# Optimization experiments

Measured on AMD Instinct MI355X. Metric: run time of the kernel, lower is better.

## Reference

```python
import jax, jax.numpy as jnp
import numpy as np

N_INPUTS = 4
ACTIVE_IDX = 0
HIDDEN = 2048
EPS = 1e-6
ROUTER_INPUT_SCALE = float(HIDDEN ** (-1.0))


def _rms_norm(x, w, eps=EPS):
    var = jnp.mean(jnp.square(x), axis=-1, keepdims=True)
    return x * jax.lax.rsqrt(var + eps) * w


def _modalities(x, w_norm, W_router):
    # tanh(router(norm(x) * hidden_size**-1)) -> [B, S, n]
    r = _rms_norm(x, w_norm) * ROUTER_INPUT_SCALE
    return jnp.tanh(r @ W_router.T)


def setup_inputs() -> dict:
    key = jax.random.key(0)
    k0, k1, k2, k3, k4 = jax.random.split(key, 5)
    B, S = 2, 4096
    return {
        "hidden_states": jax.random.normal(k0, (N_INPUTS, B, S, HIDDEN), jnp.float32),
        "activated": jax.random.normal(k1, (B, S, HIDDEN), jnp.float32),
        "w_norm": jnp.ones((HIDDEN,), jnp.float32),
        "W_router": jax.random.normal(k2, (N_INPUTS, HIDDEN), jnp.float32) * 0.02,
        "W_pred": jax.random.normal(k3, (N_INPUTS * N_INPUTS, N_INPUTS), jnp.float32) * 0.02,
        "W_corr": jax.random.normal(k4, (N_INPUTS, N_INPUTS), jnp.float32) * 0.02,
    }


def reference(hidden_states, activated, w_norm, W_router, W_pred, W_corr):
    n = N_INPUTS
    # ---- predict ----
    active = hidden_states[ACTIVE_IDX]                      # [B,S,H]
    mods = _modalities(active, w_norm, W_router)            # [B,S,n]
    coefs = (mods @ W_pred.T)                               # [B,S,n*n]
    coefs = coefs.reshape(*coefs.shape[:-1], n, n)          # [B,S,n,n]
    coefs = jnp.swapaxes(coefs, -1, -2)                     # transpose last two dims
    stacked = jnp.moveaxis(hidden_states, 0, -1)            # [B,S,H,n]
    preds = jnp.einsum('bshk,bskj->bshj', stacked, coefs) + stacked
    predictions = jnp.moveaxis(preds, -1, 0)                # [n,B,S,H]
    # ---- correct ----
    mods_c = _modalities(activated, w_norm, W_router)       # [B,S,n]
    innovation = activated - predictions[ACTIVE_IDX]        # [B,S,H]
    ccoefs = mods_c @ W_corr.T + 1.0                        # [B,S,n]
    corrected = predictions + innovation[None] * jnp.moveaxis(ccoefs, -1, 0)[..., None]
    return corrected                                        # [n,B,S,H]
```

## Files before the change

### kernel.cpp

```cpp
#include <hip/hip_runtime.h>


constexpr int H = 2048;
constexpr float EPS = 1e-6f;

__global__ __launch_bounds__(512) void altup_fused(
    const float* __restrict__ hs,
    const float* __restrict__ act,
    const float* __restrict__ w_norm,
    const float* __restrict__ W_router,
    const float* __restrict__ W_pred,
    const float* __restrict__ W_corr,
    float* __restrict__ out,
    long long T)
{
    const long long t = blockIdx.x;
    const int tid = threadIdx.x;
    const long long row = t * (long long)H;
    const long long plane = T * (long long)H;
    const int h = tid * 4;

    __shared__ float s_red[8][10];

    const float4 x0 = *reinterpret_cast<const float4*>(hs + row + h);
    const float4 x1 = *reinterpret_cast<const float4*>(hs + plane + row + h);
    const float4 x2 = *reinterpret_cast<const float4*>(hs + 2 * plane + row + h);
    const float4 x3 = *reinterpret_cast<const float4*>(hs + 3 * plane + row + h);
    const float4 xc = *reinterpret_cast<const float4*>(act + row + h);
    const float4 wn = *reinterpret_cast<const float4*>(w_norm + h);

    float p[10];
    {
        const float* a = &x0.x;
        const float* c = &xc.x;
        const float* w = &wn.x;
        float s0 = 0.f, s5 = 0.f;
#pragma unroll
        for (int e = 0; e < 4; ++e) { s0 += a[e] * a[e]; s5 += c[e] * c[e]; }
        p[0] = s0; p[5] = s5;
#pragma unroll
        for (int i = 0; i < 4; ++i) {
            const float4 wr4 = *reinterpret_cast<const float4*>(W_router + i * H + h);
            const float* r = &wr4.x;
            float da = 0.f, dc = 0.f;
#pragma unroll
            for (int e = 0; e < 4; ++e) {
                const float wre = w[e] * r[e];
                da += a[e] * wre;
                dc += c[e] * wre;
            }
            p[1 + i] = da; p[6 + i] = dc;
        }
    }

#pragma unroll
    for (int m = 1; m < 64; m <<= 1) {
#pragma unroll
        for (int i = 0; i < 10; ++i) p[i] += __shfl_xor(p[i], m, 64);
    }
    const int wave = tid >> 6;
    if ((tid & 63) == 0) {
#pragma unroll
        for (int i = 0; i < 10; ++i) s_red[wave][i] = p[i];
    }
    __syncthreads();

    float tot[10];
#pragma unroll
    for (int i = 0; i < 10; ++i) {
        float s = 0.f;
#pragma unroll
        for (int wv = 0; wv < 8; ++wv) s += s_red[wv][i];
        tot[i] = s;
    }

    const float ris = 1.0f / (float)H;
    const float inv_a = rsqrtf(tot[0] * ris + EPS) * ris;
    const float inv_c = rsqrtf(tot[5] * ris + EPS) * ris;
    float mods[4], modsc[4];
#pragma unroll
    for (int i = 0; i < 4; ++i) {
        mods[i]  = tanhf(tot[1 + i] * inv_a);
        modsc[i] = tanhf(tot[6 + i] * inv_c);
    }
    float coefT[4][4];
#pragma unroll
    for (int j = 0; j < 4; ++j)
#pragma unroll
        for (int k = 0; k < 4; ++k) {
            float s = 0.f;
#pragma unroll
            for (int m = 0; m < 4; ++m) s += mods[m] * W_pred[(j * 4 + k) * 4 + m];
            coefT[k][j] = s;
        }
    float ccoef[4];
#pragma unroll
    for (int j = 0; j < 4; ++j) {
        float s = 1.0f;
#pragma unroll
        for (int m = 0; m < 4; ++m) s += modsc[m] * W_corr[j * 4 + m];
        ccoef[j] = s;
    }

    const float* xk0 = &x0.x;
    const float* xk1 = &x1.x;
    const float* xk2 = &x2.x;
    const float* xk3 = &x3.x;
    const float* xce = &xc.x;
    float4 o4[4];
#pragma unroll
    for (int e = 0; e < 4; ++e) {
        const float xk[4] = { xk0[e], xk1[e], xk2[e], xk3[e] };
        float pred[4];
#pragma unroll
        for (int j = 0; j < 4; ++j) {
            float s = xk[j];
#pragma unroll
            for (int k = 0; k < 4; ++k) s += xk[k] * coefT[k][j];
            pred[j] = s;
        }
        const float innov = xce[e] - pred[0];
#pragma unroll
        for (int j = 0; j < 4; ++j)
            (&o4[j].x)[e] = pred[j] + innov * ccoef[j];
    }
#pragma unroll
    for (int j = 0; j < 4; ++j)
        *reinterpret_cast<float4*>(out + j * plane + row + h) = o4[j];
}

extern "C" void kernel_launch(void* const* d_in, const int* in_sizes, int n_in,
                              void* d_out, int out_size, void* d_ws, size_t ws_size,
                              hipStream_t stream) {
    const float* hs       = (const float*)d_in[0];
    const float* act      = (const float*)d_in[1];
    const float* w_norm   = (const float*)d_in[2];
    const float* W_router = (const float*)d_in[3];
    const float* W_pred   = (const float*)d_in[4];
    const float* W_corr   = (const float*)d_in[5];
    float* out = (float*)d_out;
    const long long T = (long long)in_sizes[0] / (4LL * H);
    altup_fused<<<dim3((unsigned)T), dim3(512), 0, stream>>>(
        hs, act, w_norm, W_router, W_pred, W_corr, out, T);
}
```

Before: 121.4 us.

## Split fused kernel into coefficient pass and streaming apply pass with nontemporal access

Splits the single fused kernel into two. The first computes per-token router coefficients into workspace, reading only the active plane and the activated tensor. The second streams all four planes, using nontemporal loads for planes 1-3 and nontemporal stores for the output. The intent is to keep the apply kernel lightweight and free of barriers so it runs at full bandwidth. The cost is a second launch and re-reading the active plane and activated tensor, about two extra tensor reads. The fused kernel remains as a fallback when the workspace is too small.

```diff
diff --git a/kernel.cpp b/kernel.cpp
--- a/kernel.cpp
+++ b/kernel.cpp
@@ -4,13 +4,108 @@
 constexpr int H = 2048;
 constexpr float EPS = 1e-6f;
 
-__global__ __launch_bounds__(512) void altup_fused(
+typedef float f32x4 __attribute__((ext_vector_type(4)));
+
+__global__ __launch_bounds__(512) void altup_coefs(
     const float* __restrict__ hs,
     const float* __restrict__ act,
     const float* __restrict__ w_norm,
     const float* __restrict__ W_router,
     const float* __restrict__ W_pred,
     const float* __restrict__ W_corr,
+    float* __restrict__ coefs)
+{
+    const long long t = blockIdx.x;
+    const int tid = threadIdx.x;
+    const long long row = t * (long long)H;
+    const int h = tid * 4;
+
+    __shared__ float s_red[8][10];
+
+    const f32x4 xa = *reinterpret_cast<const f32x4*>(hs + row + h);
+    const f32x4 xc = *reinterpret_cast<const f32x4*>(act + row + h);
+    const f32x4 wn = *reinterpret_cast<const f32x4*>(w_norm + h);
+
+    float p[10];
+    {
+        float s0 = 0.f, s5 = 0.f;
+#pragma unroll
+        for (int e = 0; e < 4; ++e) { s0 += xa[e] * xa[e]; s5 += xc[e] * xc[e]; }
+        p[0] = s0; p[5] = s5;
+#pragma unroll
+        for (int i = 0; i < 4; ++i) {
+            const f32x4 wr4 = *reinterpret_cast<const f32x4*>(W_router + i * H + h);
+            float da = 0.f, dc = 0.f;
+#pragma unroll
+            for (int e = 0; e < 4; ++e) {
+                const float wre = wn[e] * wr4[e];
+                da += xa[e] * wre;
+                dc += xc[e] * wre;
+            }
+            p[1 + i] = da; p[6 + i] = dc;
+        }
+    }
+
+#pragma unroll
+    for (int m = 1; m < 64; m <<= 1) {
+#pragma unroll
+        for (int i = 0; i < 10; ++i) p[i] += __shfl_xor(p[i], m, 64);
+    }
+    const int wave = tid >> 6;
+    if ((tid & 63) == 0) {
+#pragma unroll
+        for (int i = 0; i < 10; ++i) s_red[wave][i] = p[i];
+    }
+    __syncthreads();
+    if (tid != 0) return;
+
+    float tot[10];
+#pragma unroll
+    for (int i = 0; i < 10; ++i) {
+        float s = 0.f;
+#pragma unroll
+        for (int wv = 0; wv < 8; ++wv) s += s_red[wv][i];
+        tot[i] = s;
+    }
+
+    const float ris = 1.0f / (float)H;
+    const float inv_a = rsqrtf(tot[0] * ris + EPS) * ris;
+    const float inv_c = rsqrtf(tot[5] * ris + EPS) * ris;
+    float mods[4], modsc[4];
+#pragma unroll
+    for (int i = 0; i < 4; ++i) {
+        mods[i]  = tanhf(tot[1 + i] * inv_a);
+        modsc[i] = tanhf(tot[6 + i] * inv_c);
+    }
+    float cf[20];
+#pragma unroll
+    for (int k = 0; k < 4; ++k)
+#pragma unroll
+        for (int j = 0; j < 4; ++j) {
+            float s = 0.f;
+#pragma unroll
+            for (int m = 0; m < 4; ++m) s += mods[m] * W_pred[(j * 4 + k) * 4 + m];
+            cf[k * 4 + j] = s;
+        }
+#pragma unroll
+    for (int j = 0; j < 4; ++j) {
+        float s = 1.0f;
+#pragma unroll
+        for (int m = 0; m < 4; ++m) s += modsc[m] * W_corr[j * 4 + m];
+        cf[16 + j] = s;
+    }
+    float* dst = coefs + t * 20;
+#pragma unroll
+    for (int q = 0; q < 5; ++q) {
+        f32x4 v = { cf[q * 4], cf[q * 4 + 1], cf[q * 4 + 2], cf[q * 4 + 3] };
+        *reinterpret_cast<f32x4*>(dst + q * 4) = v;
+    }
+}
+
+__global__ __launch_bounds__(512) void altup_apply(
+    const float* __restrict__ hs,
+    const float* __restrict__ act,
+    const float* __restrict__ coefs,
     float* __restrict__ out,
     long long T)
 {
@@ -20,39 +115,80 @@
     const long long plane = T * (long long)H;
     const int h = tid * 4;
 
+    const f32x4 x0 = *reinterpret_cast<const f32x4*>(hs + row + h);
+    const f32x4 x1 = __builtin_nontemporal_load(
+        reinterpret_cast<const f32x4*>(hs + plane + row + h));
+    const f32x4 x2 = __builtin_nontemporal_load(
+        reinterpret_cast<const f32x4*>(hs + 2 * plane + row + h));
+    const f32x4 x3 = __builtin_nontemporal_load(
+        reinterpret_cast<const f32x4*>(hs + 3 * plane + row + h));
+    const f32x4 xc = *reinterpret_cast<const f32x4*>(act + row + h);
+
+    const float* cf = coefs + t * 20;
+    float coefT[16], ccoef[4];
+#pragma unroll
+    for (int i = 0; i < 16; ++i) coefT[i] = cf[i];
+#pragma unroll
+    for (int j = 0; j < 4; ++j) ccoef[j] = cf[16 + j];
+
+    f32x4 o4[4];
+#pragma unroll
+    for (int e = 0; e < 4; ++e) {
+        const float xk[4] = { x0[e], x1[e], x2[e], x3[e] };
+        float pred[4];
+#pragma unroll
+        for (int j = 0; j < 4; ++j) {
+            float s = xk[j];
+#pragma unroll
+            for (int k = 0; k < 4; ++k) s += xk[k] * coefT[k * 4 + j];
+            pred[j] = s;
+        }
+        const float innov = xc[e] - pred[0];
+#pragma unroll
+        for (int j = 0; j < 4; ++j)
+            o4[j][e] = pred[j] + innov * ccoef[j];
+    }
+#pragma unroll
+    for (int j = 0; j < 4; ++j)
+        __builtin_nontemporal_store(o4[j],
+            reinterpret_cast<f32x4*>(out + j * plane + row + h));
+}
+
+__global__ __launch_bounds__(512) void altup_fused(
+    const float* __restrict__ hs, const float* __restrict__ act,
+    const float* __restrict__ w_norm, const float* __restrict__ W_router,
+    const float* __restrict__ W_pred, const float* __restrict__ W_corr,
+    float* __restrict__ out, long long T)
+{
+    const long long t = blockIdx.x;
+    const int tid = threadIdx.x;
+    const long long row = t * (long long)H;
+    const long long plane = T * (long long)H;
+    const int h = tid * 4;
     __shared__ float s_red[8][10];
 
-    const float4 x0 = *reinterpret_cast<const float4*>(hs + row + h);
-    const float4 x1 = *reinterpret_cast<const float4*>(hs + plane + row + h);
-    const float4 x2 = *reinterpret_cast<const float4*>(hs + 2 * plane + row + h);
-    const float4 x3 = *reinterpret_cast<const float4*>(hs + 3 * plane + row + h);
-    const float4 xc = *reinterpret_cast<const float4*>(act + row + h);
-    const float4 wn = *reinterpret_cast<const float4*>(w_norm + h);
+    const f32x4 x0 = *reinterpret_cast<const f32x4*>(hs + row + h);
+    const f32x4 x1 = *reinterpret_cast<const f32x4*>(hs + plane + row + h);
+    const f32x4 x2 = *reinterpret_cast<const f32x4*>(hs + 2 * plane + row + h);
+    const f32x4 x3 = *reinterpret_cast<const f32x4*>(hs + 3 * plane + row + h);
+    const f32x4 xc = *reinterpret_cast<const f32x4*>(act + row + h);
+    const f32x4 wn = *reinterpret_cast<const f32x4*>(w_norm + h);
 
     float p[10];
     {
-        const float* a = &x0.x;
-        const float* c = &xc.x;
-        const float* w = &wn.x;
         float s0 = 0.f, s5 = 0.f;
 #pragma unroll
-        for (int e = 0; e < 4; ++e) { s0 += a[e] * a[e]; s5 += c[e] * c[e]; }
+        for (int e = 0; e < 4; ++e) { s0 += x0[e]*x0[e]; s5 += xc[e]*xc[e]; }
         p[0] = s0; p[5] = s5;
 #pragma unroll
         for (int i = 0; i < 4; ++i) {
-            const float4 wr4 = *reinterpret_cast<const float4*>(W_router + i * H + h);
-            const float* r = &wr4.x;
+            const f32x4 wr4 = *reinterpret_cast<const f32x4*>(W_router + i * H + h);
             float da = 0.f, dc = 0.f;
 #pragma unroll
-            for (int e = 0; e < 4; ++e) {
-                const float wre = w[e] * r[e];
-                da += a[e] * wre;
-                dc += c[e] * wre;
-            }
-            p[1 + i] = da; p[6 + i] = dc;
-        }
-    }
-
+            for (int e = 0; e < 4; ++e) { const float wre = wn[e]*wr4[e]; da += x0[e]*wre; dc += xc[e]*wre; }
+            p[1+i] = da; p[6+i] = dc;
+        }
+    }
 #pragma unroll
     for (int m = 1; m < 64; m <<= 1) {
 #pragma unroll
@@ -64,7 +200,6 @@
         for (int i = 0; i < 10; ++i) s_red[wave][i] = p[i];
     }
     __syncthreads();
-
     float tot[10];
 #pragma unroll
     for (int i = 0; i < 10; ++i) {
@@ -73,16 +208,12 @@
         for (int wv = 0; wv < 8; ++wv) s += s_red[wv][i];
         tot[i] = s;
     }
-
     const float ris = 1.0f / (float)H;
     const float inv_a = rsqrtf(tot[0] * ris + EPS) * ris;
     const float inv_c = rsqrtf(tot[5] * ris + EPS) * ris;
     float mods[4], modsc[4];
 #pragma unroll
-    for (int i = 0; i < 4; ++i) {
-        mods[i]  = tanhf(tot[1 + i] * inv_a);
-        modsc[i] = tanhf(tot[6 + i] * inv_c);
-    }
+    for (int i = 0; i < 4; ++i) { mods[i] = tanhf(tot[1+i]*inv_a); modsc[i] = tanhf(tot[6+i]*inv_c); }
     float coefT[4][4];
 #pragma unroll
     for (int j = 0; j < 4; ++j)
@@ -90,7 +221,7 @@
         for (int k = 0; k < 4; ++k) {
             float s = 0.f;
 #pragma unroll
-            for (int m = 0; m < 4; ++m) s += mods[m] * W_pred[(j * 4 + k) * 4 + m];
+            for (int m = 0; m < 4; ++m) s += mods[m] * W_pred[(j*4+k)*4 + m];
             coefT[k][j] = s;
         }
     float ccoef[4];
@@ -98,19 +229,13 @@
     for (int j = 0; j < 4; ++j) {
         float s = 1.0f;
 #pragma unroll
-        for (int m = 0; m < 4; ++m) s += modsc[m] * W_corr[j * 4 + m];
+        for (int m = 0; m < 4; ++m) s += modsc[m] * W_corr[j*4 + m];
         ccoef[j] = s;
     }
-
-    const float* xk0 = &x0.x;
-    const float* xk1 = &x1.x;
-    const float* xk2 = &x2.x;
-    const float* xk3 = &x3.x;
-    const float* xce = &xc.x;
-    float4 o4[4];
+    f32x4 o4[4];
 #pragma unroll
     for (int e = 0; e < 4; ++e) {
-        const float xk[4] = { xk0[e], xk1[e], xk2[e], xk3[e] };
+        const float xk[4] = { x0[e], x1[e], x2[e], x3[e] };
         float pred[4];
 #pragma unroll
         for (int j = 0; j < 4; ++j) {
@@ -119,14 +244,13 @@
             for (int k = 0; k < 4; ++k) s += xk[k] * coefT[k][j];
             pred[j] = s;
         }
-        const float innov = xce[e] - pred[0];
-#pragma unroll
-        for (int j = 0; j < 4; ++j)
-            (&o4[j].x)[e] = pred[j] + innov * ccoef[j];
+        const float innov = xc[e] - pred[0];
+#pragma unroll
+        for (int j = 0; j < 4; ++j) o4[j][e] = pred[j] + innov * ccoef[j];
     }
 #pragma unroll
     for (int j = 0; j < 4; ++j)
-        *reinterpret_cast<float4*>(out + j * plane + row + h) = o4[j];
+        *reinterpret_cast<f32x4*>(out + j * plane + row + h) = o4[j];
 }
 
 extern "C" void kernel_launch(void* const* d_in, const int* in_sizes, int n_in,
@@ -140,6 +264,16 @@
     const float* W_corr   = (const float*)d_in[5];
     float* out = (float*)d_out;
     const long long T = (long long)in_sizes[0] / (4LL * H);
-    altup_fused<<<dim3((unsigned)T), dim3(512), 0, stream>>>(
-        hs, act, w_norm, W_router, W_pred, W_corr, out, T);
-}
+
+    const size_t need = (size_t)T * 20 * sizeof(float);
+    if (ws_size >= need) {
+        float* coefs = (float*)d_ws;
+        altup_coefs<<<dim3((unsigned)T), dim3(512), 0, stream>>>(
+            hs, act, w_norm, W_router, W_pred, W_corr, coefs);
+        altup_apply<<<dim3((unsigned)T), dim3(512), 0, stream>>>(
+            hs, act, coefs, out, T);
+    } else {
+        altup_fused<<<dim3((unsigned)T), dim3(512), 0, stream>>>(
+            hs, act, w_norm, W_router, W_pred, W_corr, out, T);
+    }
+}
```

Result: slower. 144.4 us (+19.0%).

## Process multiple rows per block with register prefetch and nontemporal memory ops

Applied to the files above, without the earlier changes.

Each block now loops over four rows strided by the grid size, prefetching the next row's five input vectors into registers while computing the current one. Router weights premultiplied by the norm weight are loaded once per block. Streaming loads and stores use nontemporal hints to avoid cache pollution. This costs more registers and fewer blocks, which may reduce latency hiding on an already bandwidth-bound kernel.

```diff
diff --git a/kernel.cpp b/kernel.cpp
--- a/kernel.cpp
+++ b/kernel.cpp
@@ -3,6 +3,15 @@
 
 constexpr int H = 2048;
 constexpr float EPS = 1e-6f;
+
+typedef float f32x4 __attribute__((ext_vector_type(4)));
+
+__device__ __forceinline__ f32x4 nt_load(const float* p) {
+    return __builtin_nontemporal_load(reinterpret_cast<const f32x4*>(p));
+}
+__device__ __forceinline__ void nt_store(float* p, f32x4 v) {
+    __builtin_nontemporal_store(v, reinterpret_cast<f32x4*>(p));
+}
 
 __global__ __launch_bounds__(512) void altup_fused(
     const float* __restrict__ hs,
@@ -12,121 +21,135 @@
     const float* __restrict__ W_pred,
     const float* __restrict__ W_corr,
     float* __restrict__ out,
-    long long T)
+    long long T, int iters)
 {
-    const long long t = blockIdx.x;
     const int tid = threadIdx.x;
-    const long long row = t * (long long)H;
+    const int h = tid * 4;
     const long long plane = T * (long long)H;
-    const int h = tid * 4;
+    const long long strideT = gridDim.x;
 
-    __shared__ float s_red[8][10];
+    __shared__ float s_red[2][8][10];
 
-    const float4 x0 = *reinterpret_cast<const float4*>(hs + row + h);
-    const float4 x1 = *reinterpret_cast<const float4*>(hs + plane + row + h);
-    const float4 x2 = *reinterpret_cast<const float4*>(hs + 2 * plane + row + h);
-    const float4 x3 = *reinterpret_cast<const float4*>(hs + 3 * plane + row + h);
-    const float4 xc = *reinterpret_cast<const float4*>(act + row + h);
-    const float4 wn = *reinterpret_cast<const float4*>(w_norm + h);
+    const f32x4 wn = *reinterpret_cast<const f32x4*>(w_norm + h);
+    f32x4 wrw[4];
+#pragma unroll
+    for (int i = 0; i < 4; ++i) {
+        const f32x4 wr = *reinterpret_cast<const f32x4*>(W_router + i * H + h);
+#pragma unroll
+        for (int e = 0; e < 4; ++e) wrw[i][e] = wn[e] * wr[e];
+    }
 
-    float p[10];
-    {
-        const float* a = &x0.x;
-        const float* c = &xc.x;
-        const float* w = &wn.x;
-        float s0 = 0.f, s5 = 0.f;
+    long long t = blockIdx.x;
+
+    f32x4 cx0 = nt_load(hs + t * H + h);
+    f32x4 cx1 = nt_load(hs + plane + t * H + h);
+    f32x4 cx2 = nt_load(hs + 2 * plane + t * H + h);
+    f32x4 cx3 = nt_load(hs + 3 * plane + t * H + h);
+    f32x4 cxc = nt_load(act + t * H + h);
+
+    for (int it = 0; it < iters; ++it) {
+        const long long tn = t + strideT;
+        f32x4 nx0, nx1, nx2, nx3, nxc;
+        if (it + 1 < iters) {
+            nx0 = nt_load(hs + tn * H + h);
+            nx1 = nt_load(hs + plane + tn * H + h);
+            nx2 = nt_load(hs + 2 * plane + tn * H + h);
+            nx3 = nt_load(hs + 3 * plane + tn * H + h);
+            nxc = nt_load(act + tn * H + h);
+        }
+
+        float p[10];
+        {
+            float s0 = 0.f, s5 = 0.f;
 #pragma unroll
-        for (int e = 0; e < 4; ++e) { s0 += a[e] * a[e]; s5 += c[e] * c[e]; }
-        p[0] = s0; p[5] = s5;
+            for (int e = 0; e < 4; ++e) { s0 += cx0[e] * cx0[e]; s5 += cxc[e] * cxc[e]; }
+            p[0] = s0; p[5] = s5;
+#pragma unroll
+            for (int i = 0; i < 4; ++i) {
+                float da = 0.f, dc = 0.f;
+#pragma unroll
+                for (int e = 0; e < 4; ++e) {
+                    da += cx0[e] * wrw[i][e];
+                    dc += cxc[e] * wrw[i][e];
+                }
+                p[1 + i] = da; p[6 + i] = dc;
+            }
+        }
+
+#pragma unroll
+        for (int m = 1; m < 64; m <<= 1) {
+#pragma unroll
+            for (int i = 0; i < 10; ++i) p[i] += __shfl_xor(p[i], m, 64);
+        }
+        const int buf = it & 1;
+        const int wave = tid >> 6;
+        if ((tid & 63) == 0) {
+#pragma unroll
+            for (int i = 0; i < 10; ++i) s_red[buf][wave][i] = p[i];
+        }
+        __syncthreads();
+
+        float tot[10];
+#pragma unroll
+        for (int i = 0; i < 10; ++i) {
+            float s = 0.f;
+#pragma unroll
+            for (int wv = 0; wv < 8; ++wv) s += s_red[buf][wv][i];
+            tot[i] = s;
+        }
+
+        const float ris = 1.0f / (float)H;
+        const float inv_a = rsqrtf(tot[0] * ris + EPS) * ris;
+        const float inv_c = rsqrtf(tot[5] * ris + EPS) * ris;
+        float mods[4], modsc[4];
 #pragma unroll
         for (int i = 0; i < 4; ++i) {
-            const float4 wr4 = *reinterpret_cast<const float4*>(W_router + i * H + h);
-            const float* r = &wr4.x;
-            float da = 0.f, dc = 0.f;
+            mods[i]  = tanhf(tot[1 + i] * inv_a);
+            modsc[i] = tanhf(tot[6 + i] * inv_c);
+        }
+        float coefT[4][4];
 #pragma unroll
-            for (int e = 0; e < 4; ++e) {
-                const float wre = w[e] * r[e];
-                da += a[e] * wre;
-                dc += c[e] * wre;
+        for (int j = 0; j < 4; ++j)
+#pragma unroll
+            for (int k = 0; k < 4; ++k) {
+                float s = 0.f;
+#pragma unroll
+                for (int m = 0; m < 4; ++m) s += mods[m] * W_pred[(j * 4 + k) * 4 + m];
+                coefT[k][j] = s;
             }
-            p[1 + i] = da; p[6 + i] = dc;
-        }
-    }
-
-#pragma unroll
-    for (int m = 1; m < 64; m <<= 1) {
-#pragma unroll
-        for (int i = 0; i < 10; ++i) p[i] += __shfl_xor(p[i], m, 64);
-    }
-    const int wave = tid >> 6;
-    if ((tid & 63) == 0) {
-#pragma unroll
-        for (int i = 0; i < 10; ++i) s_red[wave][i] = p[i];
-    }
-    __syncthreads();
-
-    float tot[10];
-#pragma unroll
-    for (int i = 0; i < 10; ++i) {
-        float s = 0.f;
-#pragma unroll
-        for (int wv = 0; wv < 8; ++wv) s += s_red[wv][i];
-        tot[i] = s;
-    }
-
-    const float ris = 1.0f / (float)H;
-    const float inv_a = rsqrtf(tot[0] * ris + EPS) * ris;
-    const float inv_c = rsqrtf(tot[5] * ris + EPS) * ris;
-    float mods[4], modsc[4];
-#pragma unroll
-    for (int i = 0; i < 4; ++i) {
-        mods[i]  = tanhf(tot[1 + i] * inv_a);
-        modsc[i] = tanhf(tot[6 + i] * inv_c);
-    }
-    float coefT[4][4];
-#pragma unroll
-    for (int j = 0; j < 4; ++j)
-#pragma unroll
-        for (int k = 0; k < 4; ++k) {
-            float s = 0.f;
-#pragma unroll
-            for (int m = 0; m < 4; ++m) s += mods[m] * W_pred[(j * 4 + k) * 4 + m];
-            coefT[k][j] = s;
-        }
-    float ccoef[4];
-#pragma unroll
-    for (int j = 0; j < 4; ++j) {
-        float s = 1.0f;
-#pragma unroll
-        for (int m = 0; m < 4; ++m) s += modsc[m] * W_corr[j * 4 + m];
-        ccoef[j] = s;
-    }
-
-    const float* xk0 = &x0.x;
-    const float* xk1 = &x1.x;
-    const float* xk2 = &x2.x;
-    const float* xk3 = &x3.x;
-    const float* xce = &xc.x;
-    float4 o4[4];
-#pragma unroll
-    for (int e = 0; e < 4; ++e) {
-        const float xk[4] = { xk0[e], xk1[e], xk2[e], xk3[e] };
-        float pred[4];
+        float ccoef[4];
 #pragma unroll
         for (int j = 0; j < 4; ++j) {
-            float s = xk[j];
+            float s = 1.0f;
 #pragma unroll
-            for (int k = 0; k < 4; ++k) s += xk[k] * coefT[k][j];
-            pred[j] = s;
+            for (int m = 0; m < 4; ++m) s += modsc[m] * W_corr[j * 4 + m];
+            ccoef[j] = s;
         }
-        const float innov = xce[e] - pred[0];
+
+        f32x4 o4[4];
+#pragma unroll
+        for (int e = 0; e < 4; ++e) {
+            const float xk[4] = { cx0[e], cx1[e], cx2[e], cx3[e] };
+            float pred[4];
+#pragma unroll
+            for (int j = 0; j < 4; ++j) {
+                float s = xk[j];
+#pragma unroll
+                for (int k = 0; k < 4; ++k) s += xk[k] * coefT[k][j];
+                pred[j] = s;
+            }
+            const float innov = cxc[e] - pred[0];
+#pragma unroll
+            for (int j = 0; j < 4; ++j)
+                o4[j][e] = pred[j] + innov * ccoef[j];
+        }
 #pragma unroll
         for (int j = 0; j < 4; ++j)
-            (&o4[j].x)[e] = pred[j] + innov * ccoef[j];
+            nt_store(out + j * plane + t * H + h, o4[j]);
+
+        t = tn;
+        cx0 = nx0; cx1 = nx1; cx2 = nx2; cx3 = nx3; cxc = nxc;
     }
-#pragma unroll
-    for (int j = 0; j < 4; ++j)
-        *reinterpret_cast<float4*>(out + j * plane + row + h) = o4[j];
 }
 
 extern "C" void kernel_launch(void* const* d_in, const int* in_sizes, int n_in,
@@ -140,6 +163,10 @@
     const float* W_corr   = (const float*)d_in[5];
     float* out = (float*)d_out;
     const long long T = (long long)in_sizes[0] / (4LL * H);
-    altup_fused<<<dim3((unsigned)T), dim3(512), 0, stream>>>(
-        hs, act, w_norm, W_router, W_pred, W_corr, out, T);
+
+    int iters = 4;
+    if (T % iters != 0) iters = 1;
+    const unsigned grid = (unsigned)(T / iters);
+    altup_fused<<<dim3(grid), dim3(512), 0, stream>>>(
+        hs, act, w_norm, W_router, W_pred, W_corr, out, T, iters);
 }
```

Result: slower. 140.2 us (+15.5%).

## Assign one token row per wavefront instead of one row per 512-thread block

Applied to the files above, without the earlier changes.

Each 64-lane wavefront now processes a whole 2048-element token row in 8 chunks, with 4 rows per 256-thread block. This removes the shared-memory cross-wave reduction and the __syncthreads barrier. In exchange the active plane and the activated row are read twice, once for the statistics and once for the output pass, and there is less memory parallelism per row. That second read will likely hit in cache.

```diff
diff --git a/kernel.cpp b/kernel.cpp
--- a/kernel.cpp
+++ b/kernel.cpp
@@ -2,9 +2,12 @@
 
 
 constexpr int H = 2048;
+constexpr int NCHUNK = 8;
 constexpr float EPS = 1e-6f;
 
-__global__ __launch_bounds__(512) void altup_fused(
+typedef float f32x4 __attribute__((ext_vector_type(4)));
+
+__global__ __launch_bounds__(256) void altup_wave(
     const float* __restrict__ hs,
     const float* __restrict__ act,
     const float* __restrict__ w_norm,
@@ -14,42 +17,39 @@
     float* __restrict__ out,
     long long T)
 {
-    const long long t = blockIdx.x;
-    const int tid = threadIdx.x;
+    const int lane = threadIdx.x & 63;
+    const int wv   = threadIdx.x >> 6;
+    const long long t = (long long)blockIdx.x * 4 + wv;
+    if (t >= T) return;
     const long long row = t * (long long)H;
     const long long plane = T * (long long)H;
-    const int h = tid * 4;
-
-    __shared__ float s_red[8][10];
-
-    const float4 x0 = *reinterpret_cast<const float4*>(hs + row + h);
-    const float4 x1 = *reinterpret_cast<const float4*>(hs + plane + row + h);
-    const float4 x2 = *reinterpret_cast<const float4*>(hs + 2 * plane + row + h);
-    const float4 x3 = *reinterpret_cast<const float4*>(hs + 3 * plane + row + h);
-    const float4 xc = *reinterpret_cast<const float4*>(act + row + h);
-    const float4 wn = *reinterpret_cast<const float4*>(w_norm + h);
+    const int base = lane * 4;
 
     float p[10];
-    {
-        const float* a = &x0.x;
-        const float* c = &xc.x;
-        const float* w = &wn.x;
-        float s0 = 0.f, s5 = 0.f;
 #pragma unroll
-        for (int e = 0; e < 4; ++e) { s0 += a[e] * a[e]; s5 += c[e] * c[e]; }
-        p[0] = s0; p[5] = s5;
+    for (int i = 0; i < 10; ++i) p[i] = 0.f;
+
 #pragma unroll
-        for (int i = 0; i < 4; ++i) {
-            const float4 wr4 = *reinterpret_cast<const float4*>(W_router + i * H + h);
-            const float* r = &wr4.x;
-            float da = 0.f, dc = 0.f;
+    for (int c = 0; c < NCHUNK; ++c) {
+        const int off = c * 256 + base;
+        const f32x4 xa = *reinterpret_cast<const f32x4*>(hs + row + off);
+        const f32x4 xc = *reinterpret_cast<const f32x4*>(act + row + off);
+        const f32x4 wn = *reinterpret_cast<const f32x4*>(w_norm + off);
+        f32x4 wr[4];
 #pragma unroll
-            for (int e = 0; e < 4; ++e) {
-                const float wre = w[e] * r[e];
-                da += a[e] * wre;
-                dc += c[e] * wre;
+        for (int i = 0; i < 4; ++i)
+            wr[i] = *reinterpret_cast<const f32x4*>(W_router + i * H + off);
+#pragma unroll
+        for (int e = 0; e < 4; ++e) {
+            p[0] += xa[e] * xa[e];
+            p[5] += xc[e] * xc[e];
+            const float wa = xa[e] * wn[e];
+            const float wc = xc[e] * wn[e];
+#pragma unroll
+            for (int i = 0; i < 4; ++i) {
+                p[1 + i] += wa * wr[i][e];
+                p[6 + i] += wc * wr[i][e];
             }
-            p[1 + i] = da; p[6 + i] = dc;
         }
     }
 
@@ -58,30 +58,15 @@
 #pragma unroll
         for (int i = 0; i < 10; ++i) p[i] += __shfl_xor(p[i], m, 64);
     }
-    const int wave = tid >> 6;
-    if ((tid & 63) == 0) {
-#pragma unroll
-        for (int i = 0; i < 10; ++i) s_red[wave][i] = p[i];
-    }
-    __syncthreads();
-
-    float tot[10];
-#pragma unroll
-    for (int i = 0; i < 10; ++i) {
-        float s = 0.f;
-#pragma unroll
-        for (int wv = 0; wv < 8; ++wv) s += s_red[wv][i];
-        tot[i] = s;
-    }
 
     const float ris = 1.0f / (float)H;
-    const float inv_a = rsqrtf(tot[0] * ris + EPS) * ris;
-    const float inv_c = rsqrtf(tot[5] * ris + EPS) * ris;
+    const float inv_a = rsqrtf(p[0] * ris + EPS) * ris;
+    const float inv_c = rsqrtf(p[5] * ris + EPS) * ris;
     float mods[4], modsc[4];
 #pragma unroll
     for (int i = 0; i < 4; ++i) {
-        mods[i]  = tanhf(tot[1 + i] * inv_a);
-        modsc[i] = tanhf(tot[6 + i] * inv_c);
+        mods[i]  = tanhf(p[1 + i] * inv_a);
+        modsc[i] = tanhf(p[6 + i] * inv_c);
     }
     float coefT[4][4];
 #pragma unroll
@@ -102,31 +87,35 @@
         ccoef[j] = s;
     }
 
-    const float* xk0 = &x0.x;
-    const float* xk1 = &x1.x;
-    const float* xk2 = &x2.x;
-    const float* xk3 = &x3.x;
-    const float* xce = &xc.x;
-    float4 o4[4];
 #pragma unroll
-    for (int e = 0; e < 4; ++e) {
-        const float xk[4] = { xk0[e], xk1[e], xk2[e], xk3[e] };
-        float pred[4];
+    for (int c = 0; c < NCHUNK; ++c) {
+        const int off = c * 256 + base;
+        const f32x4 x0 = *reinterpret_cast<const f32x4*>(hs + row + off);
+        const f32x4 x1 = *reinterpret_cast<const f32x4*>(hs + plane + row + off);
+        const f32x4 x2 = *reinterpret_cast<const f32x4*>(hs + 2 * plane + row + off);
+        const f32x4 x3 = *reinterpret_cast<const f32x4*>(hs + 3 * plane + row + off);
+        const f32x4 xc = *reinterpret_cast<const f32x4*>(act + row + off);
+        f32x4 o4[4];
 #pragma unroll
-        for (int j = 0; j < 4; ++j) {
-            float s = xk[j];
+        for (int e = 0; e < 4; ++e) {
+            const float xk[4] = { x0[e], x1[e], x2[e], x3[e] };
+            float pred[4];
 #pragma unroll
-            for (int k = 0; k < 4; ++k) s += xk[k] * coefT[k][j];
-            pred[j] = s;
+            for (int j = 0; j < 4; ++j) {
+                float s = xk[j];
+#pragma unroll
+                for (int k = 0; k < 4; ++k) s += xk[k] * coefT[k][j];
+                pred[j] = s;
+            }
+            const float innov = xc[e] - pred[0];
+#pragma unroll
+            for (int j = 0; j < 4; ++j)
+                o4[j][e] = pred[j] + innov * ccoef[j];
         }
-        const float innov = xce[e] - pred[0];
 #pragma unroll
         for (int j = 0; j < 4; ++j)
-            (&o4[j].x)[e] = pred[j] + innov * ccoef[j];
+            *reinterpret_cast<f32x4*>(out + j * plane + row + off) = o4[j];
     }
-#pragma unroll
-    for (int j = 0; j < 4; ++j)
-        *reinterpret_cast<float4*>(out + j * plane + row + h) = o4[j];
 }
 
 extern "C" void kernel_launch(void* const* d_in, const int* in_sizes, int n_in,
@@ -140,6 +129,8 @@
     const float* W_corr   = (const float*)d_in[5];
     float* out = (float*)d_out;
     const long long T = (long long)in_sizes[0] / (4LL * H);
-    altup_fused<<<dim3((unsigned)T), dim3(512), 0, stream>>>(
+
+    const unsigned grid = (unsigned)((T + 3) / 4);
+    altup_wave<<<dim3(grid), dim3(256), 0, stream>>>(
         hs, act, w_norm, W_router, W_pred, W_corr, out, T);
 }
```

New measurement: 139.3 us. 1.15x slower.
